# Performance work log

Measured on AMD Instinct MI355X. Metric: run time of the kernel, lower is better.

## Reference

```python
import jax, jax.numpy as jnp
import numpy as np

IN_UNITS = 2048
OUT_UNITS = 2048
HIDDEN = 10
BATCH = 4096


def setup_inputs() -> dict:
    key = jax.random.key(0)
    ks = jax.random.split(key, 8)
    d = IN_UNITS + OUT_UNITS
    X = jax.random.normal(ks[0], (BATCH, IN_UNITS), dtype=jnp.float32)
    # original init is zeros (requires_grad=False); use small random weights so the
    # local rule sees non-degenerate inputs
    W = jax.random.normal(ks[1], (IN_UNITS, OUT_UNITS), dtype=jnp.float32) * 0.02
    W1 = jax.random.normal(ks[2], (d, HIDDEN), dtype=jnp.float32) / np.sqrt(d)
    b1 = jax.random.normal(ks[3], (HIDDEN,), dtype=jnp.float32) * 0.01
    W2 = jax.random.normal(ks[4], (HIDDEN, HIDDEN), dtype=jnp.float32) / np.sqrt(HIDDEN)
    b2 = jax.random.normal(ks[5], (HIDDEN,), dtype=jnp.float32) * 0.01
    W3 = jax.random.normal(ks[6], (HIDDEN, 1), dtype=jnp.float32) / np.sqrt(HIDDEN)
    b3 = jax.random.normal(ks[7], (1,), dtype=jnp.float32) * 0.01
    return {"X": X, "W": W, "W1": W1, "b1": b1, "W2": W2, "b2": b2, "W3": W3, "b3": b3}


def reference(X, W, W1, b1, W2, b2, W3, b3):
    in_u, out_u = W.shape
    # NCA local rule over all (i,j) pairs (prop_cells_updated = 1.0), batched:
    # feature for pair (i,j) is concat(W[i,:], W[:,j]) of length out_u+in_u.
    # First linear layer split so we never materialize the [in,out,in+out] tensor:
    # h1[i,j] = W[i,:] @ W1[:out_u] + W[:,j] @ W1[out_u:] + b1
    A = W @ W1[:out_u]              # [in_u, HIDDEN] row-feature contribution
    B = W.T @ W1[out_u:]            # [out_u, HIDDEN] col-feature contribution
    h = jax.nn.relu(A[:, None, :] + B[None, :, :] + b1)  # [in_u, out_u, HIDDEN]
    h = jax.nn.relu(h @ W2 + b2)                         # [in_u, out_u, HIDDEN]
    delta = (h @ W3)[..., 0] + b3[0]                     # [in_u, out_u]
    W_new = W + delta
    return jax.nn.softmax(X @ W_new, axis=-1)
```

## Files before the change

### kernel.cpp

```cpp
#include <hip/hip_runtime.h>
#include <hip/hip_fp16.h>
#include <cstdint>

#define IN_U 2048
#define OUT_U 2048
#define NH 10
#define BATCH 4096

typedef _Float16 f16;
typedef _Float16 f16x8 __attribute__((ext_vector_type(8)));
typedef float f32x4 __attribute__((ext_vector_type(4)));

__global__ __launch_bounds__(256) void k_prep(const float* __restrict__ W,
                                              const float* __restrict__ W1,
                                              const float* __restrict__ X,
                                              float* __restrict__ A,
                                              float* __restrict__ Bp,
                                              f16* __restrict__ X16) {
  __shared__ float red[4 * 64 * NH];
  int blk = blockIdx.x;
  int tid = threadIdx.x;
  int lane = tid & 63;
  int wv = tid >> 6;

  if (blk < 512) {
    int i = blk * 4 + wv;
    float acc[NH];
#pragma unroll
    for (int h = 0; h < NH; ++h) acc[h] = 0.f;
    const float* wrow = W + (size_t)i * OUT_U;
    for (int k0 = lane * 4; k0 < OUT_U; k0 += 256) {
      float4 w4 = *(const float4*)(wrow + k0);
#pragma unroll
      for (int e = 0; e < 4; ++e) {
        float wval = (&w4.x)[e];
        const float* w1r = W1 + (size_t)(k0 + e) * NH;
#pragma unroll
        for (int h = 0; h < NH; ++h) acc[h] = fmaf(wval, w1r[h], acc[h]);
      }
    }
#pragma unroll
    for (int off = 32; off > 0; off >>= 1) {
#pragma unroll
      for (int h = 0; h < NH; ++h) acc[h] += __shfl_xor(acc[h], off, 64);
    }
    if (lane == 0) {
#pragma unroll
      for (int h = 0; h < NH; ++h) A[(size_t)i * NH + h] = acc[h];
    }
  } else if (blk < 768) {
    int pb = blk - 512;
    int jt = pb & 31, kc = pb >> 5;
    int j = jt * 64 + lane;
    float acc[NH];
#pragma unroll
    for (int h = 0; h < NH; ++h) acc[h] = 0.f;
    const float* w1b = W1 + (size_t)OUT_U * NH;
    int k0 = kc * 256 + wv * 64;
#pragma unroll 4
    for (int k = k0; k < k0 + 64; ++k) {
      float wval = W[(size_t)k * OUT_U + j];
      const float* w1r = w1b + (size_t)k * NH;
#pragma unroll
      for (int h = 0; h < NH; ++h) acc[h] = fmaf(wval, w1r[h], acc[h]);
    }
#pragma unroll
    for (int h = 0; h < NH; ++h) red[wv * 640 + lane * NH + h] = acc[h];
    __syncthreads();
    for (int v = tid; v < 640; v += 256) {
      float s = red[v] + red[640 + v] + red[1280 + v] + red[1920 + v];
      Bp[(size_t)kc * (OUT_U * NH) + jt * 640 + v] = s;
    }
  } else {
    int idx = (blk - 768) * 256 + tid;
    const float4* src = (const float4*)X;
    float4 a = src[idx * 2];
    float4 b = src[idx * 2 + 1];
    f16x8 o;
    o[0] = (f16)a.x; o[1] = (f16)a.y; o[2] = (f16)a.z; o[3] = (f16)a.w;
    o[4] = (f16)b.x; o[5] = (f16)b.y; o[6] = (f16)b.z; o[7] = (f16)b.w;
    *((f16x8*)X16 + idx) = o;
  }
}

__global__ __launch_bounds__(256) void k_wnew(const float* __restrict__ W,
                                              const float* __restrict__ A,
                                              const float* __restrict__ Bp,
                                              const float* __restrict__ b1,
                                              const float* __restrict__ W2,
                                              const float* __restrict__ b2,
                                              const float* __restrict__ W3,
                                              const float* __restrict__ b3,
                                              f16* __restrict__ WnT) {
  __shared__ float Wt[64 * 65];
  __shared__ float As[64 * NH];
  __shared__ float Bs[64 * NH];
  __shared__ float W2s[NH * NH];
  __shared__ float b1s[NH], b2s[NH], w3s[NH];
  int tid = threadIdx.x;
  int i0 = blockIdx.x * 64, j0 = blockIdx.y * 64;
#pragma unroll
  for (int it = 0; it < 16; ++it) {
    int idx = it * 256 + tid;
    int r = idx >> 6, c = idx & 63;
    Wt[c * 65 + r] = W[(size_t)(i0 + r) * OUT_U + j0 + c];
  }
  for (int v = tid; v < 64 * NH; v += 256) {
    As[v] = A[(size_t)i0 * NH + v];
    float s = 0.f;
#pragma unroll
    for (int kc = 0; kc < 8; ++kc) s += Bp[(size_t)kc * (OUT_U * NH) + (size_t)j0 * NH + v];
    Bs[v] = s;
  }
  if (tid < NH * NH) W2s[tid] = W2[tid];
  if (tid < NH) { b1s[tid] = b1[tid]; b2s[tid] = b2[tid]; w3s[tid] = W3[tid]; }
  __syncthreads();

  int lane = tid & 63, w = tid >> 6;
  float b3v = b3[0];
  float ar[NH];
#pragma unroll
  for (int h = 0; h < NH; ++h) ar[h] = As[lane * NH + h] + b1s[h];

#pragma unroll
  for (int g = 0; g < 4; ++g) {
    int jb = w * 16 + g * 4;
    float h1[4][NH], s2[4][NH];
#pragma unroll
    for (int u = 0; u < 4; ++u)
#pragma unroll
      for (int p = 0; p < NH; ++p)
        h1[u][p] = fmaxf(ar[p] + Bs[(jb + u) * NH + p], 0.f);
#pragma unroll
    for (int u = 0; u < 4; ++u)
#pragma unroll
      for (int q = 0; q < NH; ++q) s2[u][q] = b2s[q];
#pragma unroll
    for (int p = 0; p < NH; ++p) {
#pragma unroll
      for (int q = 0; q < NH; ++q) {
        float wv2 = W2s[p * NH + q];
#pragma unroll
        for (int u = 0; u < 4; ++u) s2[u][q] = fmaf(h1[u][p], wv2, s2[u][q]);
      }
    }
#pragma unroll
    for (int u = 0; u < 4; ++u) {
      float d = b3v;
#pragma unroll
      for (int q = 0; q < NH; ++q) d = fmaf(fmaxf(s2[u][q], 0.f), w3s[q], d);
      float wn = Wt[(jb + u) * 65 + lane] + d;
      WnT[(size_t)(j0 + jb + u) * IN_U + i0 + lane] = (f16)wn;
    }
  }
}

__device__ __forceinline__ void gld_lds16(const void* g, void* l) {
  __builtin_amdgcn_global_load_lds((const __attribute__((address_space(1))) uint32_t*)g,
                                   (__attribute__((address_space(3))) uint32_t*)l, 16, 0, 0);
}

__global__ __launch_bounds__(256) void k_gemm(const f16* __restrict__ Am,
                                              const f16* __restrict__ Bt,
                                              float* __restrict__ C) {
  constexpr int K = IN_U;
  constexpr int N = OUT_U;
  constexpr int NKT = K / 32;
  __shared__ f16 Asl[2][128 * 32];
  __shared__ f16 Bsl[2][128 * 32];
  int tid = threadIdx.x;
  int lane = tid & 63;
  int w = tid >> 6;
  int wr = w >> 1, wc = w & 1;

  int orig = blockIdx.x;
  int swz = (orig & 7) * 64 + (orig >> 3);
  int bm = swz >> 4;
  int bn = swz & 15;

  int srow = w * 16 + (lane >> 2);
  int scol = (lane & 3) * 8;
  const f16* srcA0 = Am + (size_t)(bm * 128 + srow) * K + scol;
  const f16* srcA1 = srcA0 + (size_t)64 * K;
  const f16* srcB0 = Bt + (size_t)(bn * 128 + srow) * K + scol;
  const f16* srcB1 = srcB0 + (size_t)64 * K;

  f32x4 acc[4][4];
#pragma unroll
  for (int m = 0; m < 4; ++m)
#pragma unroll
    for (int n = 0; n < 4; ++n) acc[m][n] = (f32x4){0.f, 0.f, 0.f, 0.f};

  int rdA = (wr * 64 + (lane & 15)) * 32 + (lane >> 4) * 8;
  int rdB = (wc * 64 + (lane & 15)) * 32 + (lane >> 4) * 8;

  gld_lds16(srcA0, &Asl[0][w * 512]);
  gld_lds16(srcA1, &Asl[0][2048 + w * 512]);
  gld_lds16(srcB0, &Bsl[0][w * 512]);
  gld_lds16(srcB1, &Bsl[0][2048 + w * 512]);
  srcA0 += 32; srcA1 += 32; srcB0 += 32; srcB1 += 32;
  __syncthreads();

  for (int kt = 0; kt < NKT; ++kt) {
    int cur = kt & 1;
    if (kt + 1 < NKT) {
      gld_lds16(srcA0, &Asl[cur ^ 1][w * 512]);
      gld_lds16(srcA1, &Asl[cur ^ 1][2048 + w * 512]);
      gld_lds16(srcB0, &Bsl[cur ^ 1][w * 512]);
      gld_lds16(srcB1, &Bsl[cur ^ 1][2048 + w * 512]);
      srcA0 += 32; srcA1 += 32; srcB0 += 32; srcB1 += 32;
    }
    f16x8 af[4], bf[4];
#pragma unroll
    for (int m = 0; m < 4; ++m) af[m] = *(const f16x8*)(&Asl[cur][rdA + m * 16 * 32]);
#pragma unroll
    for (int n = 0; n < 4; ++n) bf[n] = *(const f16x8*)(&Bsl[cur][rdB + n * 16 * 32]);
#pragma unroll
    for (int m = 0; m < 4; ++m)
#pragma unroll
      for (int n = 0; n < 4; ++n)
        acc[m][n] = __builtin_amdgcn_mfma_f32_16x16x32_f16(af[m], bf[n], acc[m][n], 0, 0, 0);
    __syncthreads();
  }

  int r0 = bm * 128 + wr * 64 + (lane >> 4) * 4;
  int c0 = bn * 128 + wc * 64 + (lane & 15);
#pragma unroll
  for (int m = 0; m < 4; ++m)
#pragma unroll
    for (int n = 0; n < 4; ++n)
#pragma unroll
      for (int v = 0; v < 4; ++v)
        C[(size_t)(r0 + m * 16 + v) * N + c0 + n * 16] = acc[m][n][v];
}

__global__ __launch_bounds__(256) void k_softmax(float* __restrict__ L) {
  __shared__ float sred[4];
  int tid = threadIdx.x;
  int lane = tid & 63, w = tid >> 6;
  float4* Lr = (float4*)(L + (size_t)blockIdx.x * OUT_U);
  float4 v0 = Lr[tid];
  float4 v1 = Lr[tid + 256];
  float m = fmaxf(fmaxf(fmaxf(v0.x, v0.y), fmaxf(v0.z, v0.w)),
                  fmaxf(fmaxf(v1.x, v1.y), fmaxf(v1.z, v1.w)));
#pragma unroll
  for (int off = 32; off > 0; off >>= 1) m = fmaxf(m, __shfl_xor(m, off, 64));
  if (lane == 0) sred[w] = m;
  __syncthreads();
  m = fmaxf(fmaxf(sred[0], sred[1]), fmaxf(sred[2], sred[3]));
  __syncthreads();
  v0.x = __expf(v0.x - m); v0.y = __expf(v0.y - m);
  v0.z = __expf(v0.z - m); v0.w = __expf(v0.w - m);
  v1.x = __expf(v1.x - m); v1.y = __expf(v1.y - m);
  v1.z = __expf(v1.z - m); v1.w = __expf(v1.w - m);
  float s = v0.x + v0.y + v0.z + v0.w + v1.x + v1.y + v1.z + v1.w;
#pragma unroll
  for (int off = 32; off > 0; off >>= 1) s += __shfl_xor(s, off, 64);
  if (lane == 0) sred[w] = s;
  __syncthreads();
  s = sred[0] + sred[1] + sred[2] + sred[3];
  float inv = 1.f / s;
  v0.x *= inv; v0.y *= inv; v0.z *= inv; v0.w *= inv;
  v1.x *= inv; v1.y *= inv; v1.z *= inv; v1.w *= inv;
  Lr[tid] = v0;
  Lr[tid + 256] = v1;
}

extern "C" void kernel_launch(void* const* d_in, const int* in_sizes, int n_in,
                              void* d_out, int out_size, void* d_ws, size_t ws_size,
                              hipStream_t stream) {
  const float* X  = (const float*)d_in[0];
  const float* W  = (const float*)d_in[1];
  const float* W1 = (const float*)d_in[2];
  const float* b1 = (const float*)d_in[3];
  const float* W2 = (const float*)d_in[4];
  const float* b2 = (const float*)d_in[5];
  const float* W3 = (const float*)d_in[6];
  const float* b3 = (const float*)d_in[7];
  float* out = (float*)d_out;

  uint8_t* ws = (uint8_t*)d_ws;
  float* A   = (float*)ws;
  float* Bp  = (float*)(ws + 81920);
  f16*   X16 = (f16*)(ws + 737280);
  f16*   WnT = (f16*)(ws + 737280 + 16777216);

  hipLaunchKernelGGL(k_prep, dim3(4864), dim3(256), 0, stream, W, W1, X, A, Bp, X16);
  hipLaunchKernelGGL(k_wnew, dim3(32, 32), dim3(256), 0, stream, W, A, Bp, b1, W2, b2, W3, b3, WnT);
  hipLaunchKernelGGL(k_gemm, dim3(512), dim3(256), 0, stream, X16, WnT, out);
  hipLaunchKernelGGL(k_softmax, dim3(4096), dim3(256), 0, stream, out);
}
```

Baseline: 230.7 us.

## Rework GEMM with 32x32x16 MFMA, BK=64 and XOR-swizzled LDS tiles

The main GEMM moves from 16x16x32 MFMA with a double-buffered BK=32 tile to 32x32x16 MFMA with a single-buffered BK=64 tile, using XOR-swizzled LDS placement to avoid bank conflicts. The goal is fewer LDS reads per MFMA and fewer barriers per unit of K. In exchange the load-compute overlap from double buffering is lost, since each K-step now waits on its own load. The prep kernel also reads W1 rows as float2, and the rule kernel's group loop is no longer unrolled, which reduces register pressure.

New measurement: 240.1 us. 4.1% more time.

```diff
diff --git a/kernel.cpp b/kernel.cpp
--- a/kernel.cpp
+++ b/kernel.cpp
@@ -10,6 +10,7 @@
 typedef _Float16 f16;
 typedef _Float16 f16x8 __attribute__((ext_vector_type(8)));
 typedef float f32x4 __attribute__((ext_vector_type(4)));
+typedef float f32x16 __attribute__((ext_vector_type(16)));
 
 __global__ __launch_bounds__(256) void k_prep(const float* __restrict__ W,
                                               const float* __restrict__ W1,
@@ -34,9 +35,13 @@
 #pragma unroll
       for (int e = 0; e < 4; ++e) {
         float wval = (&w4.x)[e];
-        const float* w1r = W1 + (size_t)(k0 + e) * NH;
-#pragma unroll
-        for (int h = 0; h < NH; ++h) acc[h] = fmaf(wval, w1r[h], acc[h]);
+        const float2* w1p = (const float2*)(W1 + (size_t)(k0 + e) * NH);
+        float2 p0 = w1p[0], p1 = w1p[1], p2 = w1p[2], p3 = w1p[3], p4 = w1p[4];
+        acc[0] = fmaf(wval, p0.x, acc[0]); acc[1] = fmaf(wval, p0.y, acc[1]);
+        acc[2] = fmaf(wval, p1.x, acc[2]); acc[3] = fmaf(wval, p1.y, acc[3]);
+        acc[4] = fmaf(wval, p2.x, acc[4]); acc[5] = fmaf(wval, p2.y, acc[5]);
+        acc[6] = fmaf(wval, p3.x, acc[6]); acc[7] = fmaf(wval, p3.y, acc[7]);
+        acc[8] = fmaf(wval, p4.x, acc[8]); acc[9] = fmaf(wval, p4.y, acc[9]);
       }
     }
 #pragma unroll
@@ -60,9 +65,13 @@
 #pragma unroll 4
     for (int k = k0; k < k0 + 64; ++k) {
       float wval = W[(size_t)k * OUT_U + j];
-      const float* w1r = w1b + (size_t)k * NH;
-#pragma unroll
-      for (int h = 0; h < NH; ++h) acc[h] = fmaf(wval, w1r[h], acc[h]);
+      const float2* w1p = (const float2*)(w1b + (size_t)k * NH);
+      float2 p0 = w1p[0], p1 = w1p[1], p2 = w1p[2], p3 = w1p[3], p4 = w1p[4];
+      acc[0] = fmaf(wval, p0.x, acc[0]); acc[1] = fmaf(wval, p0.y, acc[1]);
+      acc[2] = fmaf(wval, p1.x, acc[2]); acc[3] = fmaf(wval, p1.y, acc[3]);
+      acc[4] = fmaf(wval, p2.x, acc[4]); acc[5] = fmaf(wval, p2.y, acc[5]);
+      acc[6] = fmaf(wval, p3.x, acc[6]); acc[7] = fmaf(wval, p3.y, acc[7]);
+      acc[8] = fmaf(wval, p4.x, acc[8]); acc[9] = fmaf(wval, p4.y, acc[9]);
     }
 #pragma unroll
     for (int h = 0; h < NH; ++h) red[wv * 640 + lane * NH + h] = acc[h];
@@ -122,7 +131,7 @@
 #pragma unroll
   for (int h = 0; h < NH; ++h) ar[h] = As[lane * NH + h] + b1s[h];
 
-#pragma unroll
+#pragma unroll 1
   for (int g = 0; g < 4; ++g) {
     int jb = w * 16 + g * 4;
     float h1[4][NH], s2[4][NH];
@@ -165,9 +174,10 @@
                                               float* __restrict__ C) {
   constexpr int K = IN_U;
   constexpr int N = OUT_U;
-  constexpr int NKT = K / 32;
-  __shared__ f16 Asl[2][128 * 32];
-  __shared__ f16 Bsl[2][128 * 32];
+  constexpr int BK = 64;
+  constexpr int NKT = K / BK;
+  __shared__ f16 Asl[128 * BK];
+  __shared__ f16 Bsl[128 * BK];
   int tid = threadIdx.x;
   int lane = tid & 63;
   int w = tid >> 6;
@@ -178,60 +188,63 @@
   int bm = swz >> 4;
   int bn = swz & 15;
 
-  int srow = w * 16 + (lane >> 2);
-  int scol = (lane & 3) * 8;
-  const f16* srcA0 = Am + (size_t)(bm * 128 + srow) * K + scol;
-  const f16* srcA1 = srcA0 + (size_t)64 * K;
-  const f16* srcB0 = Bt + (size_t)(bn * 128 + srow) * K + scol;
-  const f16* srcB1 = srcB0 + (size_t)64 * K;
-
-  f32x4 acc[4][4];
-#pragma unroll
-  for (int m = 0; m < 4; ++m)
-#pragma unroll
-    for (int n = 0; n < 4; ++n) acc[m][n] = (f32x4){0.f, 0.f, 0.f, 0.f};
-
-  int rdA = (wr * 64 + (lane & 15)) * 32 + (lane >> 4) * 8;
-  int rdB = (wc * 64 + (lane & 15)) * 32 + (lane >> 4) * 8;
-
-  gld_lds16(srcA0, &Asl[0][w * 512]);
-  gld_lds16(srcA1, &Asl[0][2048 + w * 512]);
-  gld_lds16(srcB0, &Bsl[0][w * 512]);
-  gld_lds16(srcB1, &Bsl[0][2048 + w * 512]);
-  srcA0 += 32; srcA1 += 32; srcB0 += 32; srcB1 += 32;
-  __syncthreads();
+  int srow = lane >> 3;
+  int schunk = (lane & 7) ^ srow;
+  const f16* sA = Am + (size_t)(bm * 128 + w * 32 + srow) * K + schunk * 8;
+  const f16* sB = Bt + (size_t)(bn * 128 + w * 32 + srow) * K + schunk * 8;
+  f16* dA = Asl + w * 32 * BK;
+  f16* dB = Bsl + w * 32 * BK;
+
+  f32x16 acc[2][2];
+#pragma unroll
+  for (int mi = 0; mi < 2; ++mi)
+#pragma unroll
+    for (int ni = 0; ni < 2; ++ni) acc[mi][ni] = (f32x16)(0.f);
+
+  int arow = wr * 64 + (lane & 31);
+  int brow = wc * 64 + (lane & 31);
+  int kgrp = lane >> 5;
+  int rswz = lane & 7;
 
   for (int kt = 0; kt < NKT; ++kt) {
-    int cur = kt & 1;
-    if (kt + 1 < NKT) {
-      gld_lds16(srcA0, &Asl[cur ^ 1][w * 512]);
-      gld_lds16(srcA1, &Asl[cur ^ 1][2048 + w * 512]);
-      gld_lds16(srcB0, &Bsl[cur ^ 1][w * 512]);
-      gld_lds16(srcB1, &Bsl[cur ^ 1][2048 + w * 512]);
-      srcA0 += 32; srcA1 += 32; srcB0 += 32; srcB1 += 32;
-    }
-    f16x8 af[4], bf[4];
-#pragma unroll
-    for (int m = 0; m < 4; ++m) af[m] = *(const f16x8*)(&Asl[cur][rdA + m * 16 * 32]);
-#pragma unroll
-    for (int n = 0; n < 4; ++n) bf[n] = *(const f16x8*)(&Bsl[cur][rdB + n * 16 * 32]);
-#pragma unroll
-    for (int m = 0; m < 4; ++m)
-#pragma unroll
-      for (int n = 0; n < 4; ++n)
-        acc[m][n] = __builtin_amdgcn_mfma_f32_16x16x32_f16(af[m], bf[n], acc[m][n], 0, 0, 0);
+#pragma unroll
+    for (int i = 0; i < 4; ++i) {
+      gld_lds16(sA + (size_t)i * 8 * K, dA + i * 8 * BK);
+      gld_lds16(sB + (size_t)i * 8 * K, dB + i * 8 * BK);
+    }
+    sA += BK; sB += BK;
     __syncthreads();
-  }
-
-  int r0 = bm * 128 + wr * 64 + (lane >> 4) * 4;
-  int c0 = bn * 128 + wc * 64 + (lane & 15);
-#pragma unroll
-  for (int m = 0; m < 4; ++m)
-#pragma unroll
-    for (int n = 0; n < 4; ++n)
-#pragma unroll
-      for (int v = 0; v < 4; ++v)
-        C[(size_t)(r0 + m * 16 + v) * N + c0 + n * 16] = acc[m][n][v];
+
+    f16x8 af[2][4], bf[2][4];
+#pragma unroll
+    for (int mi = 0; mi < 2; ++mi)
+#pragma unroll
+      for (int ks = 0; ks < 4; ++ks) {
+        int pc = (ks * 2 + kgrp) ^ rswz;
+        af[mi][ks] = *(const f16x8*)(Asl + (size_t)(arow + mi * 32) * BK + pc * 8);
+        bf[mi][ks] = *(const f16x8*)(Bsl + (size_t)(brow + mi * 32) * BK + pc * 8);
+      }
+#pragma unroll
+    for (int ks = 0; ks < 4; ++ks)
+#pragma unroll
+      for (int mi = 0; mi < 2; ++mi)
+#pragma unroll
+        for (int ni = 0; ni < 2; ++ni)
+          acc[mi][ni] = __builtin_amdgcn_mfma_f32_32x32x16_f16(af[mi][ks], bf[ni][ks], acc[mi][ni], 0, 0, 0);
+    __syncthreads();
+  }
+
+  int c0 = bn * 128 + wc * 64 + (lane & 31);
+  int r0 = bm * 128 + wr * 64 + (lane >> 5) * 4;
+#pragma unroll
+  for (int mi = 0; mi < 2; ++mi)
+#pragma unroll
+    for (int ni = 0; ni < 2; ++ni)
+#pragma unroll
+      for (int v = 0; v < 16; ++v) {
+        int row = r0 + mi * 32 + (v & 3) + 8 * (v >> 2);
+        C[(size_t)row * N + c0 + ni * 32] = acc[mi][ni][v];
+      }
 }
 
 __global__ __launch_bounds__(256) void k_softmax(float* __restrict__ L) {
```
